# Performance work log

Hardware: AMD Instinct MI355X
Metric: run time of the kernel (lower is better)

The kernel has to match this reference:

```python
import jax, jax.numpy as jnp
import numpy as np

B, N, D = 16, 4096, 256
S = 8            # num_slots
ITERS = 3
H = 256          # mlp hidden = max(dim, 256)
SCALE = D ** -0.5
TEMP = 1.0
LN_EPS = 1e-5


def _ln(x, g, b):
    mu = jnp.mean(x, axis=-1, keepdims=True)
    var = jnp.var(x, axis=-1, keepdims=True)
    return (x - mu) * jax.lax.rsqrt(var + LN_EPS) * g + b


def setup_inputs() -> dict:
    key = jax.random.key(0)
    ks = jax.random.split(key, 16)
    xav = float(np.sqrt(6.0 / (S * D + D)))  # xavier_uniform over (1,S,D)
    lin = float(np.sqrt(1.0 / D))
    return {
        "embeddings": jax.random.normal(ks[0], (B, N, D), jnp.float32),
        "slots_noise": jax.random.normal(ks[1], (1, S, D), jnp.float32) * 0.0 + jax.random.normal(ks[1], (B, S, D), jnp.float32),
        "slots_mu": jax.random.uniform(ks[2], (1, S, D), jnp.float32, -xav, xav),
        "slots_logsigma": jax.random.uniform(ks[3], (1, S, D), jnp.float32, -xav, xav),
        "Wk": jax.random.uniform(ks[4], (S, D, D), jnp.float32, -lin, lin),
        "Wq": jax.random.uniform(ks[5], (D, D), jnp.float32, -lin, lin),
        "Wv": jax.random.uniform(ks[6], (S, D, D), jnp.float32, -lin, lin),
        "W_ih": jax.random.uniform(ks[7], (3 * D, D), jnp.float32, -lin, lin),
        "W_hh": jax.random.uniform(ks[8], (3 * D, D), jnp.float32, -lin, lin),
        "b_ih": jax.random.uniform(ks[9], (3 * D,), jnp.float32, -lin, lin),
        "b_hh": jax.random.uniform(ks[10], (3 * D,), jnp.float32, -lin, lin),
        "W1": jax.random.uniform(ks[11], (H, D), jnp.float32, -lin, lin),
        "b1": jnp.zeros((H,), jnp.float32),
        "W2": jax.random.uniform(ks[12], (D, H), jnp.float32, -float(np.sqrt(1.0 / H)), float(np.sqrt(1.0 / H))),
        "b2": jnp.zeros((D,), jnp.float32),
        "g_in": jnp.ones((D,), jnp.float32), "be_in": jnp.zeros((D,), jnp.float32),
        "g_s": jnp.ones((D,), jnp.float32), "be_s": jnp.zeros((D,), jnp.float32),
        "g_ff": jnp.ones((D,), jnp.float32), "be_ff": jnp.zeros((D,), jnp.float32),
    }


def _gru(x, h, W_ih, W_hh, b_ih, b_hh):
    # torch.nn.GRUCell math; x,h: [M, D]
    gi = x @ W_ih.T + b_ih
    gh = h @ W_hh.T + b_hh
    i_r, i_z, i_n = jnp.split(gi, 3, axis=-1)
    h_r, h_z, h_n = jnp.split(gh, 3, axis=-1)
    r = jax.nn.sigmoid(i_r + h_r)
    z = jax.nn.sigmoid(i_z + h_z)
    n = jnp.tanh(i_n + r * h_n)
    return (1.0 - z) * n + z * h


def reference(embeddings, slots_noise, slots_mu, slots_logsigma, Wk, Wq, Wv,
              W_ih, W_hh, b_ih, b_hh, W1, b1, W2, b2,
              g_in, be_in, g_s, be_s, g_ff, be_ff):
    b, n, d = embeddings.shape
    slots = slots_mu + jnp.exp(slots_logsigma) * slots_noise   # [B,S,D]
    emb = _ln(embeddings, g_in, be_in)                          # [B,N,D]
    # per-slot keys / values: keys[s] = emb @ Wk[s].T  -> [S,B,N,D]
    keys = jnp.einsum('bnd,sed->sbne', emb, Wk)
    values = jnp.einsum('bnd,sed->sbne', emb, Wv)

    attn_vis = None
    for _ in range(ITERS):
        slots_prev = slots
        slots_n = _ln(slots, g_s, be_s)
        q = jnp.einsum('bsd,ed->bse', slots_n, Wq)              # [B,S,D]
        dots = jnp.einsum('bsd,sbnd->bsn', q, keys) * SCALE     # [B,S,N]
        attn = jax.nn.softmax(dots / TEMP, axis=1)              # softmax over slots
        attn_vis = attn
        attn_w = attn / jnp.sum(attn, axis=-1, keepdims=True)   # normalize over tokens
        updates = jnp.einsum('sbnd,bsn->bsd', values, attn_w)   # [B,S,D]
        h = _gru(updates.reshape(b * S, d), slots_prev.reshape(b * S, d),
                 W_ih, W_hh, b_ih, b_hh).reshape(b, S, d)
        ff = _ln(h, g_ff, be_ff)
        slots = h + (jax.nn.relu(ff @ W1.T + b1) @ W2.T + b2)
    return slots, attn_vis
```

## Files before the change

### kernel.cpp

```cpp
#include <hip/hip_runtime.h>

#define DEVI __device__ __forceinline__

constexpr float SCALE = 0.0625f;
constexpr float LN_EPS = 1e-5f;

DEVI float dot8f(const float* __restrict__ w, const float* __restrict__ x){
  float4 a = *(const float4*)w;
  float4 b = *(const float4*)(w + 4);
  return a.x*x[0]+a.y*x[1]+a.z*x[2]+a.w*x[3]+b.x*x[4]+b.y*x[5]+b.z*x[6]+b.w*x[7];
}

DEVI float gemv256_w(const float* __restrict__ W, const float* __restrict__ xv,
                     float (*part)[33], int tid){
  const int c8 = tid & 31, dp = tid >> 5;
  float xs8[8];
  #pragma unroll
  for (int j = 0; j < 8; ++j) xs8[j] = xv[c8*8 + j];
  #pragma unroll
  for (int di = 0; di < 8; ++di){
    int d = dp*8 + di;
    part[d][c8] = dot8f(W + (size_t)d*256 + c8*8, xs8);
  }
  __syncthreads();
  float acc = 0.f;
  if (tid < 256){
    #pragma unroll
    for (int p = 0; p < 32; ++p) acc += part[tid][p];
  }
  __syncthreads();
  return acc;
}

DEVI float block_ln2(float x, const float* __restrict__ g, const float* __restrict__ be,
                     float* red, int tid){
  const int lane = tid & 63, wv = tid >> 6;
  float v1 = x, v2 = x*x;
  #pragma unroll
  for (int o = 32; o; o >>= 1){ v1 += __shfl_xor(v1,o,64); v2 += __shfl_xor(v2,o,64); }
  if (tid < 256 && lane == 0){ red[wv] = v1; red[4+wv] = v2; }
  __syncthreads();
  float mu = (red[0]+red[1]+red[2]+red[3]) * (1.f/256.f);
  float var = (red[4]+red[5]+red[6]+red[7]) * (1.f/256.f) - mu*mu;
  float inv = rsqrtf(var + LN_EPS);
  float r = 0.f;
  if (tid < 256) r = (x - mu)*inv*g[tid] + be[tid];
  __syncthreads();
  return r;
}

DEVI void q_gen(float snew, int r, int s, int tid,
                const float* __restrict__ Wq, const float* __restrict__ Wk,
                const float* __restrict__ g_s, const float* __restrict__ be_s,
                const float* __restrict__ g_in, const float* __restrict__ be_in,
                float* __restrict__ qg, float* __restrict__ gqbq,
                float* xv, float (*part)[33], float (*partK)[256], float* red){
  float sn = block_ln2(snew, g_s, be_s, red, tid);
  if (tid < 256) xv[tid] = sn;
  __syncthreads();
  float q = gemv256_w(Wq, xv, part, tid);
  if (tid < 256) xv[tid] = q;
  __syncthreads();
  const int c8 = tid & 31, ep = tid >> 5;
  float acc8[8];
  #pragma unroll
  for (int j = 0; j < 8; ++j) acc8[j] = 0.f;
  const float* Wb = Wk + ((size_t)s*256)*256 + c8*8;
  #pragma unroll
  for (int ei = 0; ei < 8; ++ei){
    int e = ep*8 + ei;
    const float* wp = Wb + (size_t)e*256;
    float4 wa = *(const float4*)wp;
    float4 wb = *(const float4*)(wp + 4);
    float qe = xv[e];
    acc8[0] += qe*wa.x; acc8[1] += qe*wa.y; acc8[2] += qe*wa.z; acc8[3] += qe*wa.w;
    acc8[4] += qe*wb.x; acc8[5] += qe*wb.y; acc8[6] += qe*wb.z; acc8[7] += qe*wb.w;
  }
  float* pk = &partK[ep][c8*8];
  #pragma unroll
  for (int j = 0; j < 8; ++j) pk[j] = acc8[j];
  __syncthreads();
  float vq = 0.f, vb = 0.f;
  if (tid < 256){
    float qk = 0.f;
    #pragma unroll
    for (int p = 0; p < 32; ++p) qk += partK[p][tid];
    float qgv = qk * g_in[tid] * SCALE;
    float bqv = qk * be_in[tid] * SCALE;
    qg[r*256 + tid] = qgv;
    vq = qgv; vb = bqv;
  }
  #pragma unroll
  for (int o = 32; o; o >>= 1){ vq += __shfl_xor(vq,o,64); vb += __shfl_xor(vb,o,64); }
  if (tid < 256 && (tid & 63) == 0){ red[tid>>6] = vq; red[4+(tid>>6)] = vb; }
  __syncthreads();
  if (tid == 0) gqbq[r*2+0] = red[0]+red[1]+red[2]+red[3];
  if (tid == 1) gqbq[r*2+1] = red[4]+red[5]+red[6]+red[7];
}

__global__ __launch_bounds__(1024) void k_qg0(const float* __restrict__ noise,
    const float* __restrict__ smu, const float* __restrict__ slsig,
    const float* __restrict__ Wq, const float* __restrict__ Wk,
    const float* __restrict__ g_s, const float* __restrict__ be_s,
    const float* __restrict__ g_in, const float* __restrict__ be_in,
    float* __restrict__ slots, float* __restrict__ qg, float* __restrict__ gqbq,
    float* __restrict__ uacc, float* __restrict__ Zacc){
  __shared__ float part[256][33];
  __shared__ float partK[32][256];
  __shared__ float xv[256];
  __shared__ float red[8];
  const int r = blockIdx.x, tid = threadIdx.x;
  const int s = r & 7;
  float x = 0.f;
  if (tid < 256){
    x = smu[s*256 + tid] + expf(slsig[s*256 + tid]) * noise[r*256 + tid];
    slots[r*256 + tid] = x;
    uacc[r*256 + tid] = 0.f;
  }
  if (tid == 0) Zacc[r] = 0.f;
  q_gen(x, r, s, tid, Wq, Wk, g_s, be_s, g_in, be_in, qg, gqbq, xv, part, partK, red);
}

__global__ __launch_bounds__(256) void k_main(const float* __restrict__ emb,
    const float* __restrict__ qg, const float* __restrict__ gqbq,
    const float* __restrict__ g_in, const float* __restrict__ be_in,
    float* __restrict__ uacc, float* __restrict__ Zacc,
    float* __restrict__ out_attn, int write_attn){
  __shared__ float qgL[2048];
  __shared__ float aL[512], avL[512];
  __shared__ float4 Sp4[4*8*64];
  __shared__ float red2[2][8][4];
  __shared__ float Zs[8], A2s[8], GqL[8], BqL[8];

  const int tid = threadIdx.x, lane = tid & 63, wv = tid >> 6;
  const int blk = blockIdx.x, b = blk >> 6, tile = blk & 63;
  const int n0 = tile * 64;

  {
    const float4* src = (const float4*)(qg + (size_t)b * 2048);
    float4* dst = (float4*)qgL;
    #pragma unroll
    for (int k = 0; k < 2; ++k){
      int w = tid + k*256;
      int s = w >> 6, f = w & 63, qq = f >> 3, j = f & 7;
      dst[s*64 + qq*8 + ((j + qq) & 7)] = src[w];
    }
  }
  if (tid < 8){
    GqL[tid] = gqbq[(b*8 + tid)*2 + 0];
    BqL[tid] = gqbq[(b*8 + tid)*2 + 1];
  }
  __syncthreads();

  const int qq = tid & 7;
  float zsum[8], z2sum[8];
  #pragma unroll
  for (int s = 0; s < 8; ++s){ zsum[s] = 0.f; z2sum[s] = 0.f; }

  #pragma unroll
  for (int pass = 0; pass < 2; ++pass){
    const int t = pass*32 + (tid >> 3);
    const float4* xrow = (const float4*)(emb + ((size_t)(b*4096 + n0 + t))*256 + qq*32);
    float4 xv4[8];
    #pragma unroll
    for (int j = 0; j < 8; ++j) xv4[j] = xrow[j];
    float s1 = 0.f, s2 = 0.f, acc[8];
    #pragma unroll
    for (int s = 0; s < 8; ++s) acc[s] = 0.f;
    #pragma unroll
    for (int j = 0; j < 8; ++j){
      float4 u = xv4[j];
      s1 += (u.x+u.y)+(u.z+u.w);
      s2 += u.x*u.x+u.y*u.y+u.z*u.z+u.w*u.w;
      const float* qb = qgL + qq*32 + ((j + qq) & 7)*4;
      #pragma unroll
      for (int s = 0; s < 8; ++s){
        float4 q0 = *(const float4*)(qb + s*256);
        acc[s] += u.x*q0.x + u.y*q0.y + u.z*q0.z + u.w*q0.w;
      }
    }
    #pragma unroll
    for (int o = 1; o <= 4; o <<= 1){
      s1 += __shfl_xor(s1,o,64); s2 += __shfl_xor(s2,o,64);
      #pragma unroll
      for (int s = 0; s < 8; ++s) acc[s] += __shfl_xor(acc[s],o,64);
    }
    float mu = s1 * (1.f/256.f);
    float var = s2 * (1.f/256.f) - mu*mu;
    float inv = rsqrtf(var + LN_EPS);
    float dv[8], mx = -1e30f;
    #pragma unroll
    for (int s = 0; s < 8; ++s){
      dv[s] = inv * (acc[s] - mu * GqL[s]) + BqL[s];
      mx = fmaxf(mx, dv[s]);
    }
    float den = 0.f;
    #pragma unroll
    for (int s = 0; s < 8; ++s){ dv[s] = expf(dv[s] - mx); den += dv[s]; }
    float rden = 1.f / den;
    #pragma unroll
    for (int s = 0; s < 8; ++s){
      float at = dv[s] * rden;
      float av = at * inv;
      if (qq == 0){ avL[s*64 + t] = at; aL[s*64 + t] = av; }
      float z1 = at, z2 = av * mu;
      #pragma unroll
      for (int o = 32; o; o >>= 1){ z1 += __shfl_xor(z1, o, 64); z2 += __shfl_xor(z2, o, 64); }
      zsum[s] += z1 * 0.125f;
      z2sum[s] += z2 * 0.125f;
    }
  }
  if (lane == 0){
    #pragma unroll
    for (int s = 0; s < 8; ++s){ red2[0][s][wv] = zsum[s]; red2[1][s][wv] = z2sum[s]; }
  }
  __syncthreads();
  if (tid < 8){
    Zs[tid]  = red2[0][tid][0]+red2[0][tid][1]+red2[0][tid][2]+red2[0][tid][3];
    A2s[tid] = red2[1][tid][0]+red2[1][tid][1]+red2[1][tid][2]+red2[1][tid][3];
  }
  if (write_attn){
    int s = tid >> 5, tk = tid & 31;
    #pragma unroll
    for (int p = 0; p < 2; ++p)
      out_attn[((size_t)(b*8 + s))*4096 + n0 + p*32 + tk] = avL[s*64 + p*32 + tk];
  }
  __syncthreads();
  {
    const int r4 = tid >> 6, cq = tid & 63;
    float4 S1[8];
    #pragma unroll
    for (int s = 0; s < 8; ++s) S1[s] = make_float4(0.f,0.f,0.f,0.f);
    const float4* xbase = (const float4*)(emb + ((size_t)(b*4096 + n0))*256) + cq;
    #pragma unroll 4
    for (int i = 0; i < 16; ++i){
      int t = r4 + i*4;
      float4 x4 = xbase[t*64];
      #pragma unroll
      for (int s = 0; s < 8; ++s){
        float a = aL[s*64 + t];
        S1[s].x += a*x4.x; S1[s].y += a*x4.y; S1[s].z += a*x4.z; S1[s].w += a*x4.w;
      }
    }
    #pragma unroll
    for (int s = 0; s < 8; ++s) Sp4[(r4*8 + s)*64 + cq] = S1[s];
  }
  __syncthreads();
  {
    const int c = tid;
    const float* Sp = (const float*)Sp4;
    float gc = g_in[c], bc = be_in[c];
    float* dst = uacc + ((size_t)b*8)*256 + c;
    #pragma unroll
    for (int si = 0; si < 8; ++si){
      int s = (si + blk) & 7;
      float v = Sp[(0*8+s)*256 + c] + Sp[(1*8+s)*256 + c]
              + Sp[(2*8+s)*256 + c] + Sp[(3*8+s)*256 + c];
      atomicAdd(&dst[s*256], gc * (v - A2s[s]) + bc * Zs[s]);
    }
    if (tid < 8) atomicAdd(&Zacc[b*8 + tid], Zs[tid]);
  }
}

__global__ __launch_bounds__(1024) void k_fused(
    float* __restrict__ slots, float* __restrict__ uacc, float* __restrict__ Zacc,
    const float* __restrict__ Wv,
    const float* __restrict__ W_ih, const float* __restrict__ W_hh,
    const float* __restrict__ b_ih, const float* __restrict__ b_hh,
    const float* __restrict__ W1, const float* __restrict__ b1,
    const float* __restrict__ W2, const float* __restrict__ b2,
    const float* __restrict__ g_ff, const float* __restrict__ be_ff,
    const float* __restrict__ Wq, const float* __restrict__ Wk,
    const float* __restrict__ g_s, const float* __restrict__ be_s,
    const float* __restrict__ g_in, const float* __restrict__ be_in,
    float* __restrict__ qg, float* __restrict__ gqbq,
    float* __restrict__ out_slots, int last){
  __shared__ float part[256][33];
  __shared__ float partK[32][256];
  __shared__ float xv[256];
  __shared__ float red[8];
  __shared__ float zsh;
  const int r = blockIdx.x, tid = threadIdx.x;
  const int s = r & 7;

  float u = 0.f, hp = 0.f;
  if (tid < 256){
    u = uacc[r*256 + tid];
    uacc[r*256 + tid] = 0.f;
    xv[tid] = u;
  }
  if (tid == 0){ zsh = Zacc[r]; Zacc[r] = 0.f; }
  __syncthreads();
  const float rz = 1.f / zsh;
  float upd = gemv256_w(Wv + (size_t)s*65536, xv, part, tid) * rz;

  if (tid < 256) xv[tid] = upd;
  __syncthreads();
  float i_r = gemv256_w(W_ih,          xv, part, tid);
  float i_z = gemv256_w(W_ih +  65536, xv, part, tid);
  float i_n = gemv256_w(W_ih + 131072, xv, part, tid);

  if (tid < 256){
    hp = slots[r*256 + tid];
    xv[tid] = hp;
  }
  __syncthreads();
  float h_r = gemv256_w(W_hh,          xv, part, tid);
  float h_z = gemv256_w(W_hh +  65536, xv, part, tid);
  float h_n = gemv256_w(W_hh + 131072, xv, part, tid);

  float h = 0.f;
  if (tid < 256){
    i_r += b_ih[tid];       h_r += b_hh[tid];
    i_z += b_ih[256 + tid]; h_z += b_hh[256 + tid];
    i_n += b_ih[512 + tid]; h_n += b_hh[512 + tid];
    float rg = 1.f/(1.f + expf(-(i_r + h_r)));
    float zg = 1.f/(1.f + expf(-(i_z + h_z)));
    float ng = tanhf(i_n + rg*h_n);
    h = (1.f - zg)*ng + zg*hp;
  }
  float lnh = block_ln2(h, g_ff, be_ff, red, tid);
  if (tid < 256) xv[tid] = lnh;
  __syncthreads();
  float hid = gemv256_w(W1, xv, part, tid);
  if (tid < 256) xv[tid] = fmaxf(hid + b1[tid], 0.f);
  __syncthreads();
  float o2 = gemv256_w(W2, xv, part, tid);
  float out = 0.f;
  if (tid < 256){
    out = h + o2 + b2[tid];
    slots[r*256 + tid] = out;
    if (last) out_slots[r*256 + tid] = out;
  }
  if (last) return;
  q_gen(out, r, s, tid, Wq, Wk, g_s, be_s, g_in, be_in, qg, gqbq, xv, part, partK, red);
}

extern "C" void kernel_launch(void* const* d_in, const int* in_sizes, int n_in,
                              void* d_out, int out_size, void* d_ws, size_t ws_size,
                              hipStream_t stream){
  const float* emb   = (const float*)d_in[0];
  const float* noise = (const float*)d_in[1];
  const float* smu   = (const float*)d_in[2];
  const float* slsig = (const float*)d_in[3];
  const float* Wk    = (const float*)d_in[4];
  const float* Wq    = (const float*)d_in[5];
  const float* Wv    = (const float*)d_in[6];
  const float* W_ih  = (const float*)d_in[7];
  const float* W_hh  = (const float*)d_in[8];
  const float* b_ih  = (const float*)d_in[9];
  const float* b_hh  = (const float*)d_in[10];
  const float* W1    = (const float*)d_in[11];
  const float* b1    = (const float*)d_in[12];
  const float* W2    = (const float*)d_in[13];
  const float* b2    = (const float*)d_in[14];
  const float* g_in  = (const float*)d_in[15];
  const float* be_in = (const float*)d_in[16];
  const float* g_s   = (const float*)d_in[17];
  const float* be_s  = (const float*)d_in[18];
  const float* g_ff  = (const float*)d_in[19];
  const float* be_ff = (const float*)d_in[20];

  float* ws    = (float*)d_ws;
  float* slots = ws;
  float* qg    = ws + 32768;
  float* gqbq  = ws + 65536;
  float* uacc  = ws + 65792;
  float* Zacc  = ws + 98560;

  float* out_slots = (float*)d_out;
  float* out_attn  = out_slots + 32768;
  const int has_attn = (out_size >= 32768 + 16*8*4096);

  k_qg0<<<dim3(128), dim3(1024), 0, stream>>>(noise, smu, slsig, Wq, Wk,
      g_s, be_s, g_in, be_in, slots, qg, gqbq, uacc, Zacc);
  for (int it = 0; it < 3; ++it){
    int last = (it == 2);
    k_main<<<dim3(1024), dim3(256), 0, stream>>>(emb, qg, gqbq, g_in, be_in,
        uacc, Zacc, out_attn, last && has_attn);
    k_fused<<<dim3(128), dim3(1024), 0, stream>>>(slots, uacc, Zacc, Wv,
        W_ih, W_hh, b_ih, b_hh, W1, b1, W2, b2, g_ff, be_ff,
        Wq, Wk, g_s, be_s, g_in, be_in, qg, gqbq, out_slots, last);
  }
}
```

Measured before the change: 362.3 us.

## Restructure slot-update GEMVs into batched tiles across blocks with grid barriers

The per-row slot update used to run as 128 blocks, each doing its own chain of 256x256 GEMVs. It now runs as 128 blocks, each computing a 32-column tile for 8 rows of the same slot. Each weight tile is therefore reused across 8 rows, and the work is split by output columns instead of by row. Stages exchange data through global buffers and a software grid barrier built on atomics and spin-waiting. Slots are double-buffered across iterations, and the k_main shared memory is aliased to save LDS. The spin barrier only works if all 128 blocks are resident at once, and it adds sync latency at every stage.

Result: slower. 634.5 us (+75.1%).

```diff
diff --git a/kernel.cpp b/kernel.cpp
--- a/kernel.cpp
+++ b/kernel.cpp
@@ -4,121 +4,221 @@
 
 constexpr float SCALE = 0.0625f;
 constexpr float LN_EPS = 1e-5f;
-
-DEVI float dot8f(const float* __restrict__ w, const float* __restrict__ x){
-  float4 a = *(const float4*)w;
-  float4 b = *(const float4*)(w + 4);
-  return a.x*x[0]+a.y*x[1]+a.z*x[2]+a.w*x[3]+b.x*x[4]+b.y*x[5]+b.z*x[6]+b.w*x[7];
-}
-
-DEVI float gemv256_w(const float* __restrict__ W, const float* __restrict__ xv,
-                     float (*part)[33], int tid){
-  const int c8 = tid & 31, dp = tid >> 5;
-  float xs8[8];
+#define NBSLOT 128u
+
+DEVI void grid_barrier(unsigned* bar, unsigned target){
+  __syncthreads();
+  if (threadIdx.x == 0){
+    __threadfence();
+    __hip_atomic_fetch_add(bar, 1u, __ATOMIC_ACQ_REL, __HIP_MEMORY_SCOPE_AGENT);
+    while (__hip_atomic_load(bar, __ATOMIC_ACQUIRE, __HIP_MEMORY_SCOPE_AGENT) < target){
+      __builtin_amdgcn_s_sleep(2);
+    }
+    __threadfence();
+  }
+  __syncthreads();
+}
+
+DEVI void stage8(float* xs, const float* __restrict__ src, int rb, int tid){
+  int j = tid >> 7, k = (tid & 127) * 2;
+  *(float2*)(xs + j*256 + k) = *(const float2*)(src + (size_t)(rb + j*8)*256 + k);
+}
+
+DEVI float tile_gemm(const float* __restrict__ W, int c0, const float* xs, int tid){
+  const int out = tid >> 2, ks = tid & 3;
+  const int j = out >> 5, c = out & 31;
+  const float* wrow = W + (size_t)(c0 + c) * 256;
+  float acc = 0.f;
   #pragma unroll
-  for (int j = 0; j < 8; ++j) xs8[j] = xv[c8*8 + j];
-  #pragma unroll
-  for (int di = 0; di < 8; ++di){
-    int d = dp*8 + di;
-    part[d][c8] = dot8f(W + (size_t)d*256 + c8*8, xs8);
-  }
-  __syncthreads();
+  for (int i4 = 0; i4 < 16; ++i4){
+    int kk = ks*64 + ((i4 + 2*ks) & 15)*4;
+    float4 w = *(const float4*)(wrow + kk);
+    float4 x = *(const float4*)(xs + j*256 + kk);
+    acc += w.x*x.x + w.y*x.y + w.z*x.z + w.w*x.w;
+  }
+  acc += __shfl_xor(acc, 1, 64);
+  acc += __shfl_xor(acc, 2, 64);
+  return acc;
+}
+
+DEVI float tile_outer_qk(const float* __restrict__ Wks, int c0, const float* xs, int tid){
+  const int out = tid >> 2, ks = tid & 3;
+  const int j = out >> 5, c = out & 31;
   float acc = 0.f;
-  if (tid < 256){
-    #pragma unroll
-    for (int p = 0; p < 32; ++p) acc += part[tid][p];
-  }
-  __syncthreads();
+  #pragma unroll 8
+  for (int i = 0; i < 64; ++i){
+    int e = ks*64 + ((i + 8*ks) & 63);
+    acc += xs[j*256 + e] * Wks[(size_t)e*256 + c0 + c];
+  }
+  acc += __shfl_xor(acc, 1, 64);
+  acc += __shfl_xor(acc, 2, 64);
   return acc;
 }
 
-DEVI float block_ln2(float x, const float* __restrict__ g, const float* __restrict__ be,
-                     float* red, int tid){
-  const int lane = tid & 63, wv = tid >> 6;
-  float v1 = x, v2 = x*x;
-  #pragma unroll
-  for (int o = 32; o; o >>= 1){ v1 += __shfl_xor(v1,o,64); v2 += __shfl_xor(v2,o,64); }
-  if (tid < 256 && lane == 0){ red[wv] = v1; red[4+wv] = v2; }
-  __syncthreads();
-  float mu = (red[0]+red[1]+red[2]+red[3]) * (1.f/256.f);
-  float var = (red[4]+red[5]+red[6]+red[7]) * (1.f/256.f) - mu*mu;
-  float inv = rsqrtf(var + LN_EPS);
-  float r = 0.f;
-  if (tid < 256) r = (x - mu)*inv*g[tid] + be[tid];
-  __syncthreads();
-  return r;
-}
-
-DEVI void q_gen(float snew, int r, int s, int tid,
-                const float* __restrict__ Wq, const float* __restrict__ Wk,
-                const float* __restrict__ g_s, const float* __restrict__ be_s,
-                const float* __restrict__ g_in, const float* __restrict__ be_in,
-                float* __restrict__ qg, float* __restrict__ gqbq,
-                float* xv, float (*part)[33], float (*partK)[256], float* red){
-  float sn = block_ln2(snew, g_s, be_s, red, tid);
-  if (tid < 256) xv[tid] = sn;
-  __syncthreads();
-  float q = gemv256_w(Wq, xv, part, tid);
-  if (tid < 256) xv[tid] = q;
-  __syncthreads();
-  const int c8 = tid & 31, ep = tid >> 5;
-  float acc8[8];
-  #pragma unroll
-  for (int j = 0; j < 8; ++j) acc8[j] = 0.f;
-  const float* Wb = Wk + ((size_t)s*256)*256 + c8*8;
-  #pragma unroll
-  for (int ei = 0; ei < 8; ++ei){
-    int e = ep*8 + ei;
-    const float* wp = Wb + (size_t)e*256;
-    float4 wa = *(const float4*)wp;
-    float4 wb = *(const float4*)(wp + 4);
-    float qe = xv[e];
-    acc8[0] += qe*wa.x; acc8[1] += qe*wa.y; acc8[2] += qe*wa.z; acc8[3] += qe*wa.w;
-    acc8[4] += qe*wb.x; acc8[5] += qe*wb.y; acc8[6] += qe*wb.z; acc8[7] += qe*wb.w;
-  }
-  float* pk = &partK[ep][c8*8];
-  #pragma unroll
-  for (int j = 0; j < 8; ++j) pk[j] = acc8[j];
-  __syncthreads();
-  float vq = 0.f, vb = 0.f;
-  if (tid < 256){
-    float qk = 0.f;
-    #pragma unroll
-    for (int p = 0; p < 32; ++p) qk += partK[p][tid];
-    float qgv = qk * g_in[tid] * SCALE;
-    float bqv = qk * be_in[tid] * SCALE;
-    qg[r*256 + tid] = qgv;
-    vq = qgv; vb = bqv;
-  }
-  #pragma unroll
-  for (int o = 32; o; o >>= 1){ vq += __shfl_xor(vq,o,64); vb += __shfl_xor(vb,o,64); }
-  if (tid < 256 && (tid & 63) == 0){ red[tid>>6] = vq; red[4+(tid>>6)] = vb; }
-  __syncthreads();
-  if (tid == 0) gqbq[r*2+0] = red[0]+red[1]+red[2]+red[3];
-  if (tid == 1) gqbq[r*2+1] = red[4]+red[5]+red[6]+red[7];
-}
-
-__global__ __launch_bounds__(1024) void k_qg0(const float* __restrict__ noise,
-    const float* __restrict__ smu, const float* __restrict__ slsig,
+DEVI void ln_rows(float* xs, const float* __restrict__ g, const float* __restrict__ be,
+                  float* muL, float* invL, int tid){
+  __syncthreads();
+  if (tid < 512){
+    int j = tid >> 6, l = tid & 63;
+    float s1 = 0.f, s2 = 0.f;
+    #pragma unroll
+    for (int q = 0; q < 4; ++q){ float v = xs[j*256 + q*64 + l]; s1 += v; s2 += v*v; }
+    #pragma unroll
+    for (int o = 32; o; o >>= 1){ s1 += __shfl_xor(s1,o,64); s2 += __shfl_xor(s2,o,64); }
+    if (l == 0){
+      float mu = s1*(1.f/256.f);
+      float var = s2*(1.f/256.f) - mu*mu;
+      muL[j] = mu; invL[j] = rsqrtf(var + LN_EPS);
+    }
+  }
+  __syncthreads();
+  {
+    int j = tid >> 7, k = (tid & 127)*2;
+    float mu = muL[j], inv = invL[j];
+    float2 v = *(float2*)(xs + j*256 + k);
+    v.x = (v.x - mu)*inv*g[k]   + be[k];
+    v.y = (v.y - mu)*inv*g[k+1] + be[k+1];
+    *(float2*)(xs + j*256 + k) = v;
+  }
+  __syncthreads();
+}
+
+__global__ void k_init(const float* __restrict__ noise, const float* __restrict__ smu,
+                       const float* __restrict__ slsig, float* __restrict__ slotsA,
+                       float* __restrict__ uacc, float* __restrict__ Zacc,
+                       unsigned* __restrict__ bar){
+  const int r = blockIdx.x, tid = threadIdx.x, s = r & 7;
+  slotsA[r*256 + tid] = smu[s*256 + tid] + expf(slsig[s*256 + tid]) * noise[r*256 + tid];
+  uacc[r*256 + tid] = 0.f;
+  if (tid == 0) Zacc[r] = 0.f;
+  if (r == 0 && tid == 0) bar[0] = 0u;
+}
+
+__global__ __launch_bounds__(1024, 4) void k_slot(
+    const float* __restrict__ slots_in, float* __restrict__ slots_out,
+    float* __restrict__ uacc, float* __restrict__ Zacc,
+    const float* __restrict__ Wv,
+    const float* __restrict__ W_ih, const float* __restrict__ W_hh,
+    const float* __restrict__ b_ih, const float* __restrict__ b_hh,
+    const float* __restrict__ W1, const float* __restrict__ b1,
+    const float* __restrict__ W2, const float* __restrict__ b2,
+    const float* __restrict__ g_ff, const float* __restrict__ be_ff,
     const float* __restrict__ Wq, const float* __restrict__ Wk,
     const float* __restrict__ g_s, const float* __restrict__ be_s,
     const float* __restrict__ g_in, const float* __restrict__ be_in,
-    float* __restrict__ slots, float* __restrict__ qg, float* __restrict__ gqbq,
-    float* __restrict__ uacc, float* __restrict__ Zacc){
-  __shared__ float part[256][33];
-  __shared__ float partK[32][256];
-  __shared__ float xv[256];
-  __shared__ float red[8];
-  const int r = blockIdx.x, tid = threadIdx.x;
-  const int s = r & 7;
-  float x = 0.f;
-  if (tid < 256){
-    x = smu[s*256 + tid] + expf(slsig[s*256 + tid]) * noise[r*256 + tid];
-    slots[r*256 + tid] = x;
-    uacc[r*256 + tid] = 0.f;
-  }
-  if (tid == 0) Zacc[r] = 0.f;
-  q_gen(x, r, s, tid, Wq, Wk, g_s, be_s, g_in, be_in, qg, gqbq, xv, part, partK, red);
+    float* __restrict__ qg, float* __restrict__ gqbq,
+    float* __restrict__ upd, float* __restrict__ gh,
+    float* __restrict__ hbuf, float* __restrict__ hid, float* __restrict__ qbuf,
+    unsigned* __restrict__ bar, unsigned bar_base,
+    float* __restrict__ out_slots, int last, int initmode){
+  __shared__ float xs[8*256];
+  __shared__ float rzL[8], muL[8], invL[8];
+  const int tid = threadIdx.x;
+  const int rg = blockIdx.x >> 3, cg = blockIdx.x & 7;
+  const int s = rg & 7, bh = rg >> 3, c0 = cg*32;
+  const int rb = bh*64 + s;
+  const int out = tid >> 2, j_o = out >> 5, c_o = out & 31;
+  const int r_o = rb + j_o*8;
+  const bool own = (tid & 3) == 0;
+  unsigned bno = 0;
+
+  if (!initmode){
+    stage8(xs, uacc, rb, tid);
+    if (tid < 8) rzL[tid] = 1.f / Zacc[rb + tid*8];
+    __syncthreads();
+    {
+      float v = tile_gemm(Wv + (size_t)s*65536, c0, xs, tid);
+      if (own) upd[r_o*256 + c0 + c_o] = v * rzL[j_o];
+    }
+    __syncthreads();
+    stage8(xs, slots_in, rb, tid);
+    __syncthreads();
+    {
+      float v0 = tile_gemm(W_hh,          c0, xs, tid);
+      float v1 = tile_gemm(W_hh +  65536, c0, xs, tid);
+      float v2 = tile_gemm(W_hh + 131072, c0, xs, tid);
+      if (own){
+        gh[(0*128 + r_o)*256 + c0 + c_o] = v0;
+        gh[(1*128 + r_o)*256 + c0 + c_o] = v1;
+        gh[(2*128 + r_o)*256 + c0 + c_o] = v2;
+      }
+    }
+    grid_barrier(bar, bar_base + (++bno)*NBSLOT);
+
+    stage8(xs, upd, rb, tid);
+    __syncthreads();
+    {
+      float i0 = tile_gemm(W_ih,          c0, xs, tid);
+      float i1 = tile_gemm(W_ih +  65536, c0, xs, tid);
+      float i2 = tile_gemm(W_ih + 131072, c0, xs, tid);
+      if (own){
+        int cc = c0 + c_o;
+        float h_r = gh[(0*128 + r_o)*256 + cc] + b_hh[cc];
+        float h_z = gh[(1*128 + r_o)*256 + cc] + b_hh[256 + cc];
+        float h_n = gh[(2*128 + r_o)*256 + cc] + b_hh[512 + cc];
+        float i_r = i0 + b_ih[cc];
+        float i_z = i1 + b_ih[256 + cc];
+        float i_n = i2 + b_ih[512 + cc];
+        float hp = slots_in[r_o*256 + cc];
+        float rg_ = 1.f/(1.f + expf(-(i_r + h_r)));
+        float zg_ = 1.f/(1.f + expf(-(i_z + h_z)));
+        float ng_ = tanhf(i_n + rg_*h_n);
+        hbuf[r_o*256 + cc] = (1.f - zg_)*ng_ + zg_*hp;
+      }
+    }
+    if (tid < 256){ int jj = tid >> 5, cc = tid & 31;
+      uacc[(rb + jj*8)*256 + c0 + cc] = 0.f; }
+    if (cg == 0 && tid < 8) Zacc[rb + tid*8] = 0.f;
+    grid_barrier(bar, bar_base + (++bno)*NBSLOT);
+
+    stage8(xs, hbuf, rb, tid);
+    ln_rows(xs, g_ff, be_ff, muL, invL, tid);
+    {
+      float v = tile_gemm(W1, c0, xs, tid);
+      if (own) hid[r_o*256 + c0 + c_o] = fmaxf(v + b1[c0 + c_o], 0.f);
+    }
+    grid_barrier(bar, bar_base + (++bno)*NBSLOT);
+
+    stage8(xs, hid, rb, tid);
+    __syncthreads();
+    {
+      float v = tile_gemm(W2, c0, xs, tid);
+      if (own){
+        int cc = c0 + c_o;
+        float o = hbuf[r_o*256 + cc] + v + b2[cc];
+        slots_out[r_o*256 + cc] = o;
+        if (last) out_slots[r_o*256 + cc] = o;
+      }
+    }
+    if (last) return;
+    grid_barrier(bar, bar_base + (++bno)*NBSLOT);
+  }
+
+  stage8(xs, slots_out, rb, tid);
+  ln_rows(xs, g_s, be_s, muL, invL, tid);
+  {
+    float v = tile_gemm(Wq, c0, xs, tid);
+    if (own) qbuf[r_o*256 + c0 + c_o] = v;
+  }
+  if (cg == 0 && tid < 16) gqbq[(rb + (tid>>1)*8)*2 + (tid & 1)] = 0.f;
+  grid_barrier(bar, bar_base + (++bno)*NBSLOT);
+
+  stage8(xs, qbuf, rb, tid);
+  __syncthreads();
+  {
+    float qk = tile_outer_qk(Wk + (size_t)s*65536, c0, xs, tid);
+    int cc = c0 + c_o;
+    float qgv = qk * g_in[cc] * SCALE;
+    float bqv = qk * be_in[cc] * SCALE;
+    if (own) qg[r_o*256 + cc] = qgv;
+    float vq = own ? qgv : 0.f, vb = own ? bqv : 0.f;
+    #pragma unroll
+    for (int o = 32; o; o >>= 1){ vq += __shfl_xor(vq,o,64); vb += __shfl_xor(vb,o,64); }
+    if ((tid & 63) == 0){
+      atomicAdd(&gqbq[r_o*2 + 0], vq);
+      atomicAdd(&gqbq[r_o*2 + 1], vb);
+    }
+  }
 }
 
 __global__ __launch_bounds__(256) void k_main(const float* __restrict__ emb,
@@ -126,9 +226,11 @@
     const float* __restrict__ g_in, const float* __restrict__ be_in,
     float* __restrict__ uacc, float* __restrict__ Zacc,
     float* __restrict__ out_attn, int write_attn){
-  __shared__ float qgL[2048];
-  __shared__ float aL[512], avL[512];
-  __shared__ float4 Sp4[4*8*64];
+  __shared__ float U[8192];
+  float* const qgL = U;
+  float* const avL = U + 2048;
+  float4* const Sp4 = (float4*)U;
+  __shared__ float aL[512];
   __shared__ float red2[2][8][4];
   __shared__ float Zs[8], A2s[8], GqL[8], BqL[8];
 
@@ -260,80 +362,6 @@
     }
     if (tid < 8) atomicAdd(&Zacc[b*8 + tid], Zs[tid]);
   }
-}
-
-__global__ __launch_bounds__(1024) void k_fused(
-    float* __restrict__ slots, float* __restrict__ uacc, float* __restrict__ Zacc,
-    const float* __restrict__ Wv,
-    const float* __restrict__ W_ih, const float* __restrict__ W_hh,
-    const float* __restrict__ b_ih, const float* __restrict__ b_hh,
-    const float* __restrict__ W1, const float* __restrict__ b1,
-    const float* __restrict__ W2, const float* __restrict__ b2,
-    const float* __restrict__ g_ff, const float* __restrict__ be_ff,
-    const float* __restrict__ Wq, const float* __restrict__ Wk,
-    const float* __restrict__ g_s, const float* __restrict__ be_s,
-    const float* __restrict__ g_in, const float* __restrict__ be_in,
-    float* __restrict__ qg, float* __restrict__ gqbq,
-    float* __restrict__ out_slots, int last){
-  __shared__ float part[256][33];
-  __shared__ float partK[32][256];
-  __shared__ float xv[256];
-  __shared__ float red[8];
-  __shared__ float zsh;
-  const int r = blockIdx.x, tid = threadIdx.x;
-  const int s = r & 7;
-
-  float u = 0.f, hp = 0.f;
-  if (tid < 256){
-    u = uacc[r*256 + tid];
-    uacc[r*256 + tid] = 0.f;
-    xv[tid] = u;
-  }
-  if (tid == 0){ zsh = Zacc[r]; Zacc[r] = 0.f; }
-  __syncthreads();
-  const float rz = 1.f / zsh;
-  float upd = gemv256_w(Wv + (size_t)s*65536, xv, part, tid) * rz;
-
-  if (tid < 256) xv[tid] = upd;
-  __syncthreads();
-  float i_r = gemv256_w(W_ih,          xv, part, tid);
-  float i_z = gemv256_w(W_ih +  65536, xv, part, tid);
-  float i_n = gemv256_w(W_ih + 131072, xv, part, tid);
-
-  if (tid < 256){
-    hp = slots[r*256 + tid];
-    xv[tid] = hp;
-  }
-  __syncthreads();
-  float h_r = gemv256_w(W_hh,          xv, part, tid);
-  float h_z = gemv256_w(W_hh +  65536, xv, part, tid);
-  float h_n = gemv256_w(W_hh + 131072, xv, part, tid);
-
-  float h = 0.f;
-  if (tid < 256){
-    i_r += b_ih[tid];       h_r += b_hh[tid];
-    i_z += b_ih[256 + tid]; h_z += b_hh[256 + tid];
-    i_n += b_ih[512 + tid]; h_n += b_hh[512 + tid];
-    float rg = 1.f/(1.f + expf(-(i_r + h_r)));
-    float zg = 1.f/(1.f + expf(-(i_z + h_z)));
-    float ng = tanhf(i_n + rg*h_n);
-    h = (1.f - zg)*ng + zg*hp;
-  }
-  float lnh = block_ln2(h, g_ff, be_ff, red, tid);
-  if (tid < 256) xv[tid] = lnh;
-  __syncthreads();
-  float hid = gemv256_w(W1, xv, part, tid);
-  if (tid < 256) xv[tid] = fmaxf(hid + b1[tid], 0.f);
-  __syncthreads();
-  float o2 = gemv256_w(W2, xv, part, tid);
-  float out = 0.f;
-  if (tid < 256){
-    out = h + o2 + b2[tid];
-    slots[r*256 + tid] = out;
-    if (last) out_slots[r*256 + tid] = out;
-  }
-  if (last) return;
-  q_gen(out, r, s, tid, Wq, Wk, g_s, be_s, g_in, be_in, qg, gqbq, xv, part, partK, red);
 }
 
 extern "C" void kernel_launch(void* const* d_in, const int* in_sizes, int n_in,
@@ -361,25 +389,38 @@
   const float* g_ff  = (const float*)d_in[19];
   const float* be_ff = (const float*)d_in[20];
 
-  float* ws    = (float*)d_ws;
-  float* slots = ws;
-  float* qg    = ws + 32768;
-  float* gqbq  = ws + 65536;
-  float* uacc  = ws + 65792;
-  float* Zacc  = ws + 98560;
+  float* ws     = (float*)d_ws;
+  float* slotsA = ws;
+  float* slotsB = ws + 32768;
+  float* qg     = ws + 65536;
+  float* gqbq   = ws + 98304;
+  float* uacc   = ws + 98560;
+  float* Zacc   = ws + 131328;
+  float* upd    = ws + 131456;
+  float* gh     = ws + 164224;
+  float* hbuf   = ws + 262528;
+  float* hid    = ws + 295296;
+  float* qbuf   = ws + 328064;
+  unsigned* bar = (unsigned*)(ws + 360832);
 
   float* out_slots = (float*)d_out;
   float* out_attn  = out_slots + 32768;
   const int has_attn = (out_size >= 32768 + 16*8*4096);
 
-  k_qg0<<<dim3(128), dim3(1024), 0, stream>>>(noise, smu, slsig, Wq, Wk,
-      g_s, be_s, g_in, be_in, slots, qg, gqbq, uacc, Zacc);
+  k_init<<<dim3(128), dim3(256), 0, stream>>>(noise, smu, slsig, slotsA, uacc, Zacc, bar);
+  k_slot<<<dim3(128), dim3(1024), 0, stream>>>(slotsA, slotsA, uacc, Zacc, Wv,
+      W_ih, W_hh, b_ih, b_hh, W1, b1, W2, b2, g_ff, be_ff,
+      Wq, Wk, g_s, be_s, g_in, be_in, qg, gqbq,
+      upd, gh, hbuf, hid, qbuf, bar, 0u, out_slots, 0, 1);
   for (int it = 0; it < 3; ++it){
     int last = (it == 2);
+    float* sin  = (it == 1) ? slotsB : slotsA;
+    float* sout = (it == 1) ? slotsA : slotsB;
     k_main<<<dim3(1024), dim3(256), 0, stream>>>(emb, qg, gqbq, g_in, be_in,
         uacc, Zacc, out_attn, last && has_attn);
-    k_fused<<<dim3(128), dim3(1024), 0, stream>>>(slots, uacc, Zacc, Wv,
+    k_slot<<<dim3(128), dim3(1024), 0, stream>>>(sin, sout, uacc, Zacc, Wv,
         W_ih, W_hh, b_ih, b_hh, W1, b1, W2, b2, g_ff, be_ff,
-        Wq, Wk, g_s, be_s, g_in, be_in, qg, gqbq, out_slots, last);
-  }
-}
+        Wq, Wk, g_s, be_s, g_in, be_in, qg, gqbq,
+        upd, gh, hbuf, hid, qbuf, bar, 128u*(1u + 5u*(unsigned)it), out_slots, last, 0);
+  }
+}
```

## Split fused slot-update kernel into multiple smaller parallel kernels

Applied to the files above, without the earlier changes.

Replaces the single 1024-thread per-slot fused kernel (Wv gemv, GRU, MLP, q generation) with a chain of 256-thread kernels. The independent gemvs (Wv and the three W_hh gates, then the three W_ih gates) now run as separate blocks on a 2D grid, which raises parallelism across CUs. Slot state is double-buffered between iterations. k_main also reuses shared memory through aliasing and defers its cross-lane Z reductions until after the slot loop, cutting shuffle work. The cost is more kernel launches and extra global round-trips for the intermediate buffers.

Result: faster. 328.1 us (-9.4%).

```diff
diff --git a/kernel.cpp b/kernel.cpp
--- a/kernel.cpp
+++ b/kernel.cpp
@@ -11,64 +11,159 @@
   return a.x*x[0]+a.y*x[1]+a.z*x[2]+a.w*x[3]+b.x*x[4]+b.y*x[5]+b.z*x[6]+b.w*x[7];
 }
 
-DEVI float gemv256_w(const float* __restrict__ W, const float* __restrict__ xv,
-                     float (*part)[33], int tid){
-  const int c8 = tid & 31, dp = tid >> 5;
+DEVI float gemv256(const float* __restrict__ W, const float* __restrict__ xv,
+                   float (*part)[33], int tid){
+  const int c8 = tid & 31, ep = tid >> 5;
   float xs8[8];
   #pragma unroll
   for (int j = 0; j < 8; ++j) xs8[j] = xv[c8*8 + j];
-  #pragma unroll
-  for (int di = 0; di < 8; ++di){
-    int d = dp*8 + di;
-    part[d][c8] = dot8f(W + (size_t)d*256 + c8*8, xs8);
+  const float* Wb = W + c8*8;
+  #pragma unroll 4
+  for (int ei = 0; ei < 32; ++ei){
+    int e = ep*32 + ei;
+    part[e][c8] = dot8f(Wb + (size_t)e*256, xs8);
   }
   __syncthreads();
   float acc = 0.f;
-  if (tid < 256){
-    #pragma unroll
-    for (int p = 0; p < 32; ++p) acc += part[tid][p];
-  }
-  __syncthreads();
+  #pragma unroll
+  for (int p = 0; p < 32; ++p) acc += part[tid][p];
   return acc;
 }
 
-DEVI float block_ln2(float x, const float* __restrict__ g, const float* __restrict__ be,
-                     float* red, int tid){
-  const int lane = tid & 63, wv = tid >> 6;
+DEVI float block_ln(float x, const float* __restrict__ g, const float* __restrict__ be,
+                    float* red, int tid, int lane, int wv){
   float v1 = x, v2 = x*x;
   #pragma unroll
   for (int o = 32; o; o >>= 1){ v1 += __shfl_xor(v1,o,64); v2 += __shfl_xor(v2,o,64); }
-  if (tid < 256 && lane == 0){ red[wv] = v1; red[4+wv] = v2; }
+  if (lane == 0){ red[wv] = v1; red[4+wv] = v2; }
   __syncthreads();
   float mu = (red[0]+red[1]+red[2]+red[3]) * (1.f/256.f);
   float var = (red[4]+red[5]+red[6]+red[7]) * (1.f/256.f) - mu*mu;
   float inv = rsqrtf(var + LN_EPS);
-  float r = 0.f;
-  if (tid < 256) r = (x - mu)*inv*g[tid] + be[tid];
+  float r = (x - mu)*inv*g[tid] + be[tid];
   __syncthreads();
   return r;
 }
 
-DEVI void q_gen(float snew, int r, int s, int tid,
-                const float* __restrict__ Wq, const float* __restrict__ Wk,
-                const float* __restrict__ g_s, const float* __restrict__ be_s,
-                const float* __restrict__ g_in, const float* __restrict__ be_in,
-                float* __restrict__ qg, float* __restrict__ gqbq,
-                float* xv, float (*part)[33], float (*partK)[256], float* red){
-  float sn = block_ln2(snew, g_s, be_s, red, tid);
-  if (tid < 256) xv[tid] = sn;
-  __syncthreads();
-  float q = gemv256_w(Wq, xv, part, tid);
-  if (tid < 256) xv[tid] = q;
+__global__ void k_init(const float* __restrict__ noise, const float* __restrict__ smu,
+                       const float* __restrict__ slsig, float* __restrict__ slotsA,
+                       float* __restrict__ uacc, float* __restrict__ Zacc){
+  const int r = blockIdx.x, tid = threadIdx.x, s = r & 7;
+  slotsA[r*256 + tid] = smu[s*256 + tid] + expf(slsig[s*256 + tid]) * noise[r*256 + tid];
+  uacc[r*256 + tid] = 0.f;
+  if (tid == 0) Zacc[r] = 0.f;
+}
+
+__global__ __launch_bounds__(256) void kS1(const float* __restrict__ slots_in,
+    const float* __restrict__ uacc, const float* __restrict__ Zacc,
+    const float* __restrict__ Wv, const float* __restrict__ W_hh,
+    float* __restrict__ upd, float* __restrict__ gh){
+  __shared__ float xv[256];
+  __shared__ float part[256][33];
+  const int m = blockIdx.x;
+  const int r = blockIdx.y, tid = threadIdx.x, s = r & 7;
+  const float* W   = (m == 0) ? (Wv + (size_t)s*65536) : (W_hh + (size_t)(m-1)*65536);
+  const float* src = (m == 0) ? (uacc + r*256) : (slots_in + r*256);
+  xv[tid] = src[tid];
+  __syncthreads();
+  float acc = gemv256(W, xv, part, tid);
+  if (m == 0) upd[r*256 + tid] = acc * (1.f / Zacc[r]);
+  else        gh[((m-1)*128 + r)*256 + tid] = acc;
+}
+
+__global__ __launch_bounds__(256) void kS2(const float* __restrict__ upd,
+    const float* __restrict__ W_ih, const float* __restrict__ b_ih,
+    float* __restrict__ gi, float* __restrict__ uacc, float* __restrict__ Zacc){
+  __shared__ float xv[256];
+  __shared__ float part[256][33];
+  const int g = blockIdx.x, r = blockIdx.y, tid = threadIdx.x;
+  xv[tid] = upd[r*256 + tid];
+  if (g == 0) uacc[r*256 + tid] = 0.f;
+  if (g == 1 && tid == 0) Zacc[r] = 0.f;
+  __syncthreads();
+  float acc = gemv256(W_ih + (size_t)g*65536, xv, part, tid);
+  gi[(g*128 + r)*256 + tid] = acc + b_ih[g*256 + tid];
+}
+
+__global__ __launch_bounds__(256) void kS3(const float* __restrict__ slots_in,
+    const float* __restrict__ gi, const float* __restrict__ gh,
+    const float* __restrict__ b_hh,
+    const float* __restrict__ g_ff, const float* __restrict__ be_ff,
+    const float* __restrict__ W1, const float* __restrict__ b1,
+    float* __restrict__ hbuf, float* __restrict__ hid){
+  __shared__ float xv[256];
+  __shared__ float part[256][33];
+  __shared__ float red[8];
+  const int r = blockIdx.x, tid = threadIdx.x;
+  const int lane = tid & 63, wv = tid >> 6;
+  float i_r = gi[(0*128 + r)*256 + tid];
+  float i_z = gi[(1*128 + r)*256 + tid];
+  float i_n = gi[(2*128 + r)*256 + tid];
+  float h_r = gh[(0*128 + r)*256 + tid] + b_hh[tid];
+  float h_z = gh[(1*128 + r)*256 + tid] + b_hh[256 + tid];
+  float h_n = gh[(2*128 + r)*256 + tid] + b_hh[512 + tid];
+  float hp = slots_in[r*256 + tid];
+  float rg = 1.f/(1.f + expf(-(i_r + h_r)));
+  float zg = 1.f/(1.f + expf(-(i_z + h_z)));
+  float ng = tanhf(i_n + rg*h_n);
+  float h = (1.f - zg)*ng + zg*hp;
+  hbuf[r*256 + tid] = h;
+  float lnh = block_ln(h, g_ff, be_ff, red, tid, lane, wv);
+  xv[tid] = lnh;
+  __syncthreads();
+  float acc = gemv256(W1, xv, part, tid);
+  hid[r*256 + tid] = fmaxf(acc + b1[tid], 0.f);
+}
+
+__global__ __launch_bounds__(256) void kS4(const float* __restrict__ hid,
+    const float* __restrict__ hbuf, const float* __restrict__ W2,
+    const float* __restrict__ b2, float* __restrict__ slots_out,
+    float* __restrict__ out_slots, int last){
+  __shared__ float xv[256];
+  __shared__ float part[256][33];
+  const int r = blockIdx.x, tid = threadIdx.x;
+  xv[tid] = hid[r*256 + tid];
+  __syncthreads();
+  float acc = gemv256(W2, xv, part, tid);
+  float out = hbuf[r*256 + tid] + acc + b2[tid];
+  slots_out[r*256 + tid] = out;
+  if (last) out_slots[r*256 + tid] = out;
+}
+
+__global__ __launch_bounds__(256) void kS5(const float* __restrict__ slots,
+    const float* __restrict__ g_s, const float* __restrict__ be_s,
+    const float* __restrict__ Wq, float* __restrict__ qbuf){
+  __shared__ float xv[256];
+  __shared__ float part[256][33];
+  __shared__ float red[8];
+  const int r = blockIdx.x, tid = threadIdx.x;
+  const int lane = tid & 63, wv = tid >> 6;
+  float x = slots[r*256 + tid];
+  float sn = block_ln(x, g_s, be_s, red, tid, lane, wv);
+  xv[tid] = sn;
+  __syncthreads();
+  qbuf[r*256 + tid] = gemv256(Wq, xv, part, tid);
+}
+
+__global__ __launch_bounds__(256) void kS6(const float* __restrict__ qbuf,
+    const float* __restrict__ Wk,
+    const float* __restrict__ g_in, const float* __restrict__ be_in,
+    float* __restrict__ qg, float* __restrict__ gqbq){
+  __shared__ float xv[256];
+  __shared__ float partK[8][256];
+  __shared__ float red[8];
+  const int r = blockIdx.x, tid = threadIdx.x, s = r & 7;
+  const int lane = tid & 63, wv = tid >> 6;
+  xv[tid] = qbuf[r*256 + tid];
   __syncthreads();
   const int c8 = tid & 31, ep = tid >> 5;
   float acc8[8];
   #pragma unroll
   for (int j = 0; j < 8; ++j) acc8[j] = 0.f;
   const float* Wb = Wk + ((size_t)s*256)*256 + c8*8;
-  #pragma unroll
-  for (int ei = 0; ei < 8; ++ei){
-    int e = ep*8 + ei;
+  #pragma unroll 4
+  for (int ei = 0; ei < 32; ++ei){
+    int e = ep*32 + ei;
     const float* wp = Wb + (size_t)e*256;
     float4 wa = *(const float4*)wp;
     float4 wb = *(const float4*)(wp + 4);
@@ -80,45 +175,19 @@
   #pragma unroll
   for (int j = 0; j < 8; ++j) pk[j] = acc8[j];
   __syncthreads();
-  float vq = 0.f, vb = 0.f;
-  if (tid < 256){
-    float qk = 0.f;
-    #pragma unroll
-    for (int p = 0; p < 32; ++p) qk += partK[p][tid];
-    float qgv = qk * g_in[tid] * SCALE;
-    float bqv = qk * be_in[tid] * SCALE;
-    qg[r*256 + tid] = qgv;
-    vq = qgv; vb = bqv;
-  }
+  float qk = 0.f;
+  #pragma unroll
+  for (int p = 0; p < 8; ++p) qk += partK[p][tid];
+  float qgv = qk * g_in[tid] * SCALE;
+  float bqv = qk * be_in[tid] * SCALE;
+  qg[r*256 + tid] = qgv;
+  float vq = qgv, vb = bqv;
   #pragma unroll
   for (int o = 32; o; o >>= 1){ vq += __shfl_xor(vq,o,64); vb += __shfl_xor(vb,o,64); }
-  if (tid < 256 && (tid & 63) == 0){ red[tid>>6] = vq; red[4+(tid>>6)] = vb; }
+  if (lane == 0){ red[wv] = vq; red[4+wv] = vb; }
   __syncthreads();
   if (tid == 0) gqbq[r*2+0] = red[0]+red[1]+red[2]+red[3];
   if (tid == 1) gqbq[r*2+1] = red[4]+red[5]+red[6]+red[7];
-}
-
-__global__ __launch_bounds__(1024) void k_qg0(const float* __restrict__ noise,
-    const float* __restrict__ smu, const float* __restrict__ slsig,
-    const float* __restrict__ Wq, const float* __restrict__ Wk,
-    const float* __restrict__ g_s, const float* __restrict__ be_s,
-    const float* __restrict__ g_in, const float* __restrict__ be_in,
-    float* __restrict__ slots, float* __restrict__ qg, float* __restrict__ gqbq,
-    float* __restrict__ uacc, float* __restrict__ Zacc){
-  __shared__ float part[256][33];
-  __shared__ float partK[32][256];
-  __shared__ float xv[256];
-  __shared__ float red[8];
-  const int r = blockIdx.x, tid = threadIdx.x;
-  const int s = r & 7;
-  float x = 0.f;
-  if (tid < 256){
-    x = smu[s*256 + tid] + expf(slsig[s*256 + tid]) * noise[r*256 + tid];
-    slots[r*256 + tid] = x;
-    uacc[r*256 + tid] = 0.f;
-  }
-  if (tid == 0) Zacc[r] = 0.f;
-  q_gen(x, r, s, tid, Wq, Wk, g_s, be_s, g_in, be_in, qg, gqbq, xv, part, partK, red);
 }
 
 __global__ __launch_bounds__(256) void k_main(const float* __restrict__ emb,
@@ -126,9 +195,11 @@
     const float* __restrict__ g_in, const float* __restrict__ be_in,
     float* __restrict__ uacc, float* __restrict__ Zacc,
     float* __restrict__ out_attn, int write_attn){
-  __shared__ float qgL[2048];
-  __shared__ float aL[512], avL[512];
-  __shared__ float4 Sp4[4*8*64];
+  __shared__ float U[8192];
+  float* const qgL = U;
+  float* const avL = U + 2048;
+  float4* const Sp4 = (float4*)U;
+  __shared__ float aL[512];
   __shared__ float red2[2][8][4];
   __shared__ float Zs[8], A2s[8], GqL[8], BqL[8];
 
@@ -203,16 +274,21 @@
       float at = dv[s] * rden;
       float av = at * inv;
       if (qq == 0){ avL[s*64 + t] = at; aL[s*64 + t] = av; }
-      float z1 = at, z2 = av * mu;
-      #pragma unroll
-      for (int o = 32; o; o >>= 1){ z1 += __shfl_xor(z1, o, 64); z2 += __shfl_xor(z2, o, 64); }
-      zsum[s] += z1 * 0.125f;
-      z2sum[s] += z2 * 0.125f;
+      zsum[s] += at;
+      z2sum[s] += av * mu;
+    }
+  }
+  #pragma unroll
+  for (int s = 0; s < 8; ++s){
+    #pragma unroll
+    for (int o = 32; o; o >>= 1){
+      zsum[s] += __shfl_xor(zsum[s], o, 64);
+      z2sum[s] += __shfl_xor(z2sum[s], o, 64);
     }
   }
   if (lane == 0){
     #pragma unroll
-    for (int s = 0; s < 8; ++s){ red2[0][s][wv] = zsum[s]; red2[1][s][wv] = z2sum[s]; }
+    for (int s = 0; s < 8; ++s){ red2[0][s][wv] = zsum[s]*0.125f; red2[1][s][wv] = z2sum[s]*0.125f; }
   }
   __syncthreads();
   if (tid < 8){
@@ -260,80 +336,6 @@
     }
     if (tid < 8) atomicAdd(&Zacc[b*8 + tid], Zs[tid]);
   }
-}
-
-__global__ __launch_bounds__(1024) void k_fused(
-    float* __restrict__ slots, float* __restrict__ uacc, float* __restrict__ Zacc,
-    const float* __restrict__ Wv,
-    const float* __restrict__ W_ih, const float* __restrict__ W_hh,
-    const float* __restrict__ b_ih, const float* __restrict__ b_hh,
-    const float* __restrict__ W1, const float* __restrict__ b1,
-    const float* __restrict__ W2, const float* __restrict__ b2,
-    const float* __restrict__ g_ff, const float* __restrict__ be_ff,
-    const float* __restrict__ Wq, const float* __restrict__ Wk,
-    const float* __restrict__ g_s, const float* __restrict__ be_s,
-    const float* __restrict__ g_in, const float* __restrict__ be_in,
-    float* __restrict__ qg, float* __restrict__ gqbq,
-    float* __restrict__ out_slots, int last){
-  __shared__ float part[256][33];
-  __shared__ float partK[32][256];
-  __shared__ float xv[256];
-  __shared__ float red[8];
-  __shared__ float zsh;
-  const int r = blockIdx.x, tid = threadIdx.x;
-  const int s = r & 7;
-
-  float u = 0.f, hp = 0.f;
-  if (tid < 256){
-    u = uacc[r*256 + tid];
-    uacc[r*256 + tid] = 0.f;
-    xv[tid] = u;
-  }
-  if (tid == 0){ zsh = Zacc[r]; Zacc[r] = 0.f; }
-  __syncthreads();
-  const float rz = 1.f / zsh;
-  float upd = gemv256_w(Wv + (size_t)s*65536, xv, part, tid) * rz;
-
-  if (tid < 256) xv[tid] = upd;
-  __syncthreads();
-  float i_r = gemv256_w(W_ih,          xv, part, tid);
-  float i_z = gemv256_w(W_ih +  65536, xv, part, tid);
-  float i_n = gemv256_w(W_ih + 131072, xv, part, tid);
-
-  if (tid < 256){
-    hp = slots[r*256 + tid];
-    xv[tid] = hp;
-  }
-  __syncthreads();
-  float h_r = gemv256_w(W_hh,          xv, part, tid);
-  float h_z = gemv256_w(W_hh +  65536, xv, part, tid);
-  float h_n = gemv256_w(W_hh + 131072, xv, part, tid);
-
-  float h = 0.f;
-  if (tid < 256){
-    i_r += b_ih[tid];       h_r += b_hh[tid];
-    i_z += b_ih[256 + tid]; h_z += b_hh[256 + tid];
-    i_n += b_ih[512 + tid]; h_n += b_hh[512 + tid];
-    float rg = 1.f/(1.f + expf(-(i_r + h_r)));
-    float zg = 1.f/(1.f + expf(-(i_z + h_z)));
-    float ng = tanhf(i_n + rg*h_n);
-    h = (1.f - zg)*ng + zg*hp;
-  }
-  float lnh = block_ln2(h, g_ff, be_ff, red, tid);
-  if (tid < 256) xv[tid] = lnh;
-  __syncthreads();
-  float hid = gemv256_w(W1, xv, part, tid);
-  if (tid < 256) xv[tid] = fmaxf(hid + b1[tid], 0.f);
-  __syncthreads();
-  float o2 = gemv256_w(W2, xv, part, tid);
-  float out = 0.f;
-  if (tid < 256){
-    out = h + o2 + b2[tid];
-    slots[r*256 + tid] = out;
-    if (last) out_slots[r*256 + tid] = out;
-  }
-  if (last) return;
-  q_gen(out, r, s, tid, Wq, Wk, g_s, be_s, g_in, be_in, qg, gqbq, xv, part, partK, red);
 }
 
 extern "C" void kernel_launch(void* const* d_in, const int* in_sizes, int n_in,
@@ -361,25 +363,40 @@
   const float* g_ff  = (const float*)d_in[19];
   const float* be_ff = (const float*)d_in[20];
 
-  float* ws    = (float*)d_ws;
-  float* slots = ws;
-  float* qg    = ws + 32768;
-  float* gqbq  = ws + 65536;
-  float* uacc  = ws + 65792;
-  float* Zacc  = ws + 98560;
+  float* ws     = (float*)d_ws;
+  float* slotsA = ws;
+  float* slotsB = ws + 32768;
+  float* qg     = ws + 65536;
+  float* gqbq   = ws + 98304;
+  float* uacc   = ws + 98560;
+  float* Zacc   = ws + 131328;
+  float* upd    = ws + 131456;
+  float* gh     = ws + 164224;
+  float* gi     = ws + 262528;
+  float* hbuf   = ws + 360832;
+  float* hid    = ws + 393600;
+  float* qbuf   = ws + 426368;
 
   float* out_slots = (float*)d_out;
   float* out_attn  = out_slots + 32768;
   const int has_attn = (out_size >= 32768 + 16*8*4096);
 
-  k_qg0<<<dim3(128), dim3(1024), 0, stream>>>(noise, smu, slsig, Wq, Wk,
-      g_s, be_s, g_in, be_in, slots, qg, gqbq, uacc, Zacc);
+  k_init<<<dim3(128), dim3(256), 0, stream>>>(noise, smu, slsig, slotsA, uacc, Zacc);
+  kS5<<<dim3(128), dim3(256), 0, stream>>>(slotsA, g_s, be_s, Wq, qbuf);
+  kS6<<<dim3(128), dim3(256), 0, stream>>>(qbuf, Wk, g_in, be_in, qg, gqbq);
   for (int it = 0; it < 3; ++it){
     int last = (it == 2);
+    float* sin  = (it == 1) ? slotsB : slotsA;
+    float* sout = (it == 1) ? slotsA : slotsB;
     k_main<<<dim3(1024), dim3(256), 0, stream>>>(emb, qg, gqbq, g_in, be_in,
         uacc, Zacc, out_attn, last && has_attn);
-    k_fused<<<dim3(128), dim3(1024), 0, stream>>>(slots, uacc, Zacc, Wv,
-        W_ih, W_hh, b_ih, b_hh, W1, b1, W2, b2, g_ff, be_ff,
-        Wq, Wk, g_s, be_s, g_in, be_in, qg, gqbq, out_slots, last);
-  }
-}
+    kS1<<<dim3(4,128), dim3(256), 0, stream>>>(sin, uacc, Zacc, Wv, W_hh, upd, gh);
+    kS2<<<dim3(3,128), dim3(256), 0, stream>>>(upd, W_ih, b_ih, gi, uacc, Zacc);
+    kS3<<<dim3(128), dim3(256), 0, stream>>>(sin, gi, gh, b_hh, g_ff, be_ff, W1, b1, hbuf, hid);
+    kS4<<<dim3(128), dim3(256), 0, stream>>>(hid, hbuf, W2, b2, sout, out_slots, last);
+    if (!last){
+      kS5<<<dim3(128), dim3(256), 0, stream>>>(sout, g_s, be_s, Wq, qbuf);
+      kS6<<<dim3(128), dim3(256), 0, stream>>>(qbuf, Wk, g_in, be_in, qg, gqbq);
+    }
+  }
+}
```
